# Kernel tuning notes

Hardware: AMD Instinct MI355X
Metric: run time of the kernel (lower is better)

Reference implementation:

```python
import jax, jax.numpy as jnp
import numpy as np

B = 8            # graphs per batch (batch_size)
NPG = 4096       # nodes per graph
EPG = 65536      # edges per graph (avg degree 16)
IN = 384
K1, K2, K3 = 2458, 1475, 738   # ceil(.6*4096), ceil(.6*2458), ceil(.5*1475)
EPS = 1e-5


def setup_inputs() -> dict:
    key = jax.random.key(0)
    ks = jax.random.split(key, 16)
    x = jax.random.normal(ks[0], (B * NPG, IN), jnp.float32)
    off = (jnp.arange(B, dtype=jnp.int32) * NPG)[:, None]
    src = jax.random.randint(ks[1], (B, EPG), 0, NPG, dtype=jnp.int32) + off
    dst = jax.random.randint(ks[2], (B, EPG), 0, NPG, dtype=jnp.int32) + off
    edge_index = jnp.stack([src.reshape(-1), dst.reshape(-1)])

    def lin(k, i, o):
        return jax.random.normal(k, (i, o), jnp.float32) / np.sqrt(i)

    return dict(
        x=x, edge_index=edge_index,
        W1=lin(ks[3], IN, 512), b1=jnp.zeros(512, jnp.float32),
        W2=lin(ks[4], 512, 512), b2=jnp.zeros(512, jnp.float32),
        W3=lin(ks[5], 512, 256), b3=jnp.zeros(256, jnp.float32),
        W4=lin(ks[6], 256, 192), b4=jnp.zeros(192, jnp.float32),
        g1=jnp.ones(512, jnp.float32), be1=jnp.zeros(512, jnp.float32),
        g2=jnp.ones(512, jnp.float32), be2=jnp.zeros(512, jnp.float32),
        g3=jnp.ones(256, jnp.float32), be3=jnp.zeros(256, jnp.float32),
        p1_wrel=lin(ks[7], 512, 1), p1_brel=jnp.zeros(1, jnp.float32), p1_wroot=lin(ks[8], 512, 1),
        p2_wrel=lin(ks[9], 512, 1), p2_brel=jnp.zeros(1, jnp.float32), p2_wroot=lin(ks[10], 512, 1),
        p3_wrel=lin(ks[11], 256, 1), p3_brel=jnp.zeros(1, jnp.float32), p3_wroot=lin(ks[12], 256, 1),
    )


def _gcn_conv(x, W, b, src, dst, em, n):
    # PyG GCNConv(add_self_loops=False): h = D^-1/2 A D^-1/2 (x W) + b
    h = x @ W
    deg = jax.ops.segment_sum(em, dst, num_segments=n)           # in-degree of valid edges
    dis = jnp.where(deg > 0, jax.lax.rsqrt(jnp.maximum(deg, 1e-12)), 0.0)
    norm = (dis[src] * dis[dst] * em)[:, None]
    return jax.ops.segment_sum(h[src] * norm, dst, num_segments=n) + b


def _bn(x, g, b):
    # BatchNorm(track_running_stats=False): always batch stats, biased var
    mu = jnp.mean(x, axis=0)
    var = jnp.mean(jnp.square(x - mu), axis=0)
    return (x - mu) * jax.lax.rsqrt(var + EPS) * g + b


def _sag_score(x, wrel, brel, wroot, src, dst, em, n):
    # SAGPooling's GNN = GraphConv: lin_rel(sum_j x_j) + lin_root(x)
    agg = jax.ops.segment_sum(x[src] * em[:, None], dst, num_segments=n)
    return (agg @ wrel + brel + x @ wroot)[:, 0]


def _sag_pool(x, score, src, dst, em, npg, k):
    # per-graph top-k on raw scores; kept features scaled by tanh(score)
    topv, topi = jax.lax.top_k(score.reshape(B, npg), k)
    perm = (topi + (jnp.arange(B, dtype=jnp.int32) * npg)[:, None]).reshape(-1)
    xn = x[perm] * jnp.tanh(topv.reshape(-1))[:, None]
    inv = jnp.full(B * npg, -1, jnp.int32).at[perm].set(
        jnp.arange(B * k, dtype=jnp.int32))
    ns, nd = inv[src], inv[dst]
    keep = (ns >= 0) & (nd >= 0)
    em = em * keep.astype(x.dtype)
    return xn, jnp.where(keep, ns, 0), jnp.where(keep, nd, 0), em


def reference(x, edge_index,
              W1, b1, W2, b2, W3, b3, W4, b4,
              g1, be1, g2, be2, g3, be3,
              p1_wrel, p1_brel, p1_wroot,
              p2_wrel, p2_brel, p2_wroot,
              p3_wrel, p3_brel, p3_wroot,
              batch_size=8):
    src, dst = edge_index[0], edge_index[1]
    em = jnp.ones(src.shape[0], x.dtype)

    h = jax.nn.relu(_bn(_gcn_conv(x, W1, b1, src, dst, em, B * NPG), g1, be1))
    s = _sag_score(h, p1_wrel, p1_brel, p1_wroot, src, dst, em, B * NPG)
    h, src, dst, em = _sag_pool(h, s, src, dst, em, NPG, K1)

    h = jax.nn.relu(_bn(_gcn_conv(h, W2, b2, src, dst, em, B * K1), g2, be2))
    s = _sag_score(h, p2_wrel, p2_brel, p2_wroot, src, dst, em, B * K1)
    h, src, dst, em = _sag_pool(h, s, src, dst, em, K1, K2)

    h = jax.nn.relu(_bn(_gcn_conv(h, W3, b3, src, dst, em, B * K2), g3, be3))
    s = _sag_score(h, p3_wrel, p3_brel, p3_wroot, src, dst, em, B * K2)
    h, src, dst, em = _sag_pool(h, s, src, dst, em, K2, K3)

    h = _gcn_conv(h, W4, b4, src, dst, em, B * K3)      # [B*K3, 192]
    hg = h.reshape(B, K3, 192)
    return jnp.mean(hg, axis=1) + jnp.max(hg, axis=1)   # global mean + max pool
```

## Files before the change

kernel.cpp:

```cpp
#include <hip/hip_runtime.h>
#include <cmath>

#define E_TOTAL 524288
#define NB 8

using f32x4 = __attribute__((ext_vector_type(4))) float;
using s16x8 = __attribute__((ext_vector_type(8))) short;
using s16x4 = __attribute__((ext_vector_type(4))) short;

static inline int cdiv(int a, int b) { return (a + b - 1) / b; }

__device__ inline unsigned short bf16_rn(float x) {
  unsigned u = __float_as_uint(x);
  return (unsigned short)((u + 0x7FFFu + ((u >> 16) & 1u)) >> 16);
}
__device__ inline void split3(float x, short& h, short& m, short& l) {
  unsigned short hb = bf16_rn(x);
  h = (short)hb;
  float hf = __uint_as_float(((unsigned)hb) << 16);
  float r1 = x - hf;
  unsigned short mb = bf16_rn(r1);
  m = (short)mb;
  float mf = __uint_as_float(((unsigned)mb) << 16);
  l = (short)bf16_rn(r1 - mf);
}

__global__ void fill_i32(int* p, int v, int n) {
  int i = blockIdx.x * 256 + threadIdx.x;
  if (i < n) p[i] = v;
}

__global__ void split_w_t(const float* __restrict__ W, short* __restrict__ TH,
                          short* __restrict__ TM, short* __restrict__ TL, int K, int N) {
  int i = blockIdx.x * 256 + threadIdx.x;
  if (i >= K * N) return;
  int k = i / N, n = i % N;
  short h, m, l;
  split3(W[i], h, m, l);
  TH[(size_t)n * K + k] = h;
  TM[(size_t)n * K + k] = m;
  TL[(size_t)n * K + k] = l;
}

#define GBM 128
#define GBN 128
#define GBK 32
#define ASTR 40

__global__ __launch_bounds__(256) void gemm_mfma(
    const short* __restrict__ AH, const short* __restrict__ AM, const short* __restrict__ AL,
    const short* __restrict__ BH, const short* __restrict__ BM, const short* __restrict__ BL,
    const float* __restrict__ bias, float* __restrict__ C,
    int M, int K, int N, int nblocks) {
  __shared__ __align__(16) short Ah[GBM * ASTR];
  __shared__ __align__(16) short Am[GBM * ASTR];
  __shared__ __align__(16) short Al[GBM * ASTR];
  __shared__ __align__(16) short Bh[GBN * ASTR];
  __shared__ __align__(16) short Bm[GBN * ASTR];
  __shared__ __align__(16) short Bl[GBN * ASTR];
  int nwg = gridDim.x;
  int orig = blockIdx.x;
  int q = nwg >> 3, r = nwg & 7;
  int xc = orig & 7, j8 = orig >> 3;
  int wg = (xc < r ? xc * (q + 1) : r * (q + 1) + (xc - r) * q) + j8;
  int bm = (wg / nblocks) * GBM;
  int bn = (wg % nblocks) * GBN;
  int tid = threadIdx.x;
  int wave = tid >> 6, lane = tid & 63;
  int wm = (wave >> 1) * 64, wn = (wave & 1) * 64;
  int l15 = lane & 15, l4 = lane >> 4;
  int arow = tid >> 1, ahalf = tid & 1;
  int garow = bm + arow;
  int gbcol = bn + arow;
  const bool avalid = garow < M;
  const bool bvalid = gbcol < N;
  int sw = (arow >> 3) & 3;
  int wofs0 = arow * ASTR + (((2 * ahalf) ^ sw) << 3);
  int wofs1 = arow * ASTR + (((2 * ahalf + 1) ^ sw) << 3);
  f32x4 acc[4][4] = {};
  for (int k0 = 0; k0 < K; k0 += GBK) {
    __syncthreads();
    {
      s16x8 z = {};
      size_t ga = (size_t)garow * K + k0 + ahalf * 16;
      size_t gb = (size_t)gbcol * K + k0 + ahalf * 16;
      s16x8 v0, v1;
      v0 = avalid ? *(const s16x8*)(AH + ga) : z;
      v1 = avalid ? *(const s16x8*)(AH + ga + 8) : z;
      *(s16x8*)&Ah[wofs0] = v0;  *(s16x8*)&Ah[wofs1] = v1;
      v0 = avalid ? *(const s16x8*)(AM + ga) : z;
      v1 = avalid ? *(const s16x8*)(AM + ga + 8) : z;
      *(s16x8*)&Am[wofs0] = v0;  *(s16x8*)&Am[wofs1] = v1;
      v0 = avalid ? *(const s16x8*)(AL + ga) : z;
      v1 = avalid ? *(const s16x8*)(AL + ga + 8) : z;
      *(s16x8*)&Al[wofs0] = v0;  *(s16x8*)&Al[wofs1] = v1;
      v0 = bvalid ? *(const s16x8*)(BH + gb) : z;
      v1 = bvalid ? *(const s16x8*)(BH + gb + 8) : z;
      *(s16x8*)&Bh[wofs0] = v0;  *(s16x8*)&Bh[wofs1] = v1;
      v0 = bvalid ? *(const s16x8*)(BM + gb) : z;
      v1 = bvalid ? *(const s16x8*)(BM + gb + 8) : z;
      *(s16x8*)&Bm[wofs0] = v0;  *(s16x8*)&Bm[wofs1] = v1;
      v0 = bvalid ? *(const s16x8*)(BL + gb) : z;
      v1 = bvalid ? *(const s16x8*)(BL + gb + 8) : z;
      *(s16x8*)&Bl[wofs0] = v0;  *(s16x8*)&Bl[wofs1] = v1;
    }
    __syncthreads();
    s16x8 fah[4], fam[4], fal[4], fbh[4], fbm[4], fbl[4];
#pragma unroll
    for (int mi = 0; mi < 4; ++mi) {
      int row = wm + mi * 16 + l15;
      int ad = row * ASTR + ((l4 ^ ((row >> 3) & 3)) << 3);
      fah[mi] = *(const s16x8*)&Ah[ad];
      fam[mi] = *(const s16x8*)&Am[ad];
      fal[mi] = *(const s16x8*)&Al[ad];
    }
#pragma unroll
    for (int ni = 0; ni < 4; ++ni) {
      int row = wn + ni * 16 + l15;
      int bd = row * ASTR + ((l4 ^ ((row >> 3) & 3)) << 3);
      fbh[ni] = *(const s16x8*)&Bh[bd];
      fbm[ni] = *(const s16x8*)&Bm[bd];
      fbl[ni] = *(const s16x8*)&Bl[bd];
    }
#pragma unroll
    for (int mi = 0; mi < 4; ++mi)
#pragma unroll
      for (int ni = 0; ni < 4; ++ni) {
        acc[mi][ni] = __builtin_amdgcn_mfma_f32_16x16x32_bf16(fah[mi], fbh[ni], acc[mi][ni], 0, 0, 0);
        acc[mi][ni] = __builtin_amdgcn_mfma_f32_16x16x32_bf16(fah[mi], fbm[ni], acc[mi][ni], 0, 0, 0);
        acc[mi][ni] = __builtin_amdgcn_mfma_f32_16x16x32_bf16(fam[mi], fbh[ni], acc[mi][ni], 0, 0, 0);
        acc[mi][ni] = __builtin_amdgcn_mfma_f32_16x16x32_bf16(fah[mi], fbl[ni], acc[mi][ni], 0, 0, 0);
        acc[mi][ni] = __builtin_amdgcn_mfma_f32_16x16x32_bf16(fal[mi], fbh[ni], acc[mi][ni], 0, 0, 0);
        acc[mi][ni] = __builtin_amdgcn_mfma_f32_16x16x32_bf16(fam[mi], fbm[ni], acc[mi][ni], 0, 0, 0);
      }
  }
#pragma unroll
  for (int ni = 0; ni < 4; ++ni) {
    int col = bn + wn + ni * 16 + l15;
    if (col >= N) continue;
    float bv = bias ? bias[col] : 0.f;
#pragma unroll
    for (int mi = 0; mi < 4; ++mi) {
      int row0 = bm + wm + mi * 16 + l4 * 4;
#pragma unroll
      for (int rr = 0; rr < 4; ++rr) {
        int row = row0 + rr;
        if (row < M) C[(size_t)row * N + col] = acc[mi][ni][rr] + bv;
      }
    }
  }
}

__global__ void count_kernel(const int* __restrict__ dst, int* __restrict__ cnt, int E) {
  int e = blockIdx.x * 256 + threadIdx.x;
  if (e >= E) return;
  atomicAdd(&cnt[dst[e]], 1);
}

__global__ __launch_bounds__(1024) void scan_kernel(const int* __restrict__ cnt,
                                                    int* __restrict__ offs, int n) {
  __shared__ int tsum[1024];
  int tid = threadIdx.x;
  int chunk = (n + 1023) / 1024;
  int base = tid * chunk;
  int lsum = 0;
  for (int i = 0; i < chunk; ++i) {
    int idx = base + i;
    if (idx < n) lsum += cnt[idx];
  }
  tsum[tid] = lsum;
  __syncthreads();
  for (int off = 1; off < 1024; off <<= 1) {
    int add = (tid >= off) ? tsum[tid - off] : 0;
    __syncthreads();
    tsum[tid] += add;
    __syncthreads();
  }
  int run = (tid == 0) ? 0 : tsum[tid - 1];
  for (int i = 0; i < chunk; ++i) {
    int idx = base + i;
    if (idx < n) { offs[idx] = run; run += cnt[idx]; }
  }
  if (tid == 1023) offs[n] = run;
}

__global__ void dis_kernel(const int* __restrict__ cnt, float* __restrict__ dis, int n) {
  int i = blockIdx.x * 256 + threadIdx.x;
  if (i >= n) return;
  int c = cnt[i];
  dis[i] = (c > 0) ? (float)(1.0 / sqrt((double)c)) : 0.f;
}

__global__ void scatter_kernel(const int* __restrict__ src, const int* __restrict__ dst,
                               const int* __restrict__ offs, int* __restrict__ tmpc,
                               int* __restrict__ esrc, int E) {
  int e = blockIdx.x * 256 + threadIdx.x;
  if (e >= E) return;
  int d = dst[e];
  if (d < 0) return;
  int pos = offs[d] + atomicAdd(&tmpc[d], 1);
  esrc[pos] = src[e];
}

__global__ void sort_buckets(const int* __restrict__ offs, int* __restrict__ esrc, int n) {
  int node = blockIdx.x * 256 + threadIdx.x;
  if (node >= n) return;
  int s0 = offs[node], s1 = offs[node + 1];
  for (int i = s0 + 1; i < s1; ++i) {
    int v = esrc[i];
    int j = i - 1;
    while (j >= s0 && esrc[j] > v) { esrc[j + 1] = esrc[j]; --j; }
    esrc[j + 1] = v;
  }
}

__global__ __launch_bounds__(256) void agg_kernel(
    const float* __restrict__ h, const int* __restrict__ offs,
    const int* __restrict__ esrc, const float* __restrict__ dis,
    const float* __restrict__ bias, float* __restrict__ outf,
    short* __restrict__ outh, short* __restrict__ outm, short* __restrict__ outl,
    int F, int n) {
  int node = blockIdx.x * 4 + (threadIdx.x >> 6);
  if (node >= n) return;
  int lane = threadIdx.x & 63;
  int nf4 = F >> 2;
  int i0 = lane, i1 = lane + 64;
  bool a0 = i0 < nf4, a1 = i1 < nf4;
  f32x4 acc0 = {}, acc1 = {};
  int e0 = offs[node], e1 = offs[node + 1];
  int e = e0;
  for (; e + 4 <= e1; e += 4) {
    int s0 = esrc[e], s1 = esrc[e + 1], s2 = esrc[e + 2], s3 = esrc[e + 3];
    float w0 = dis[s0], w1 = dis[s1], w2 = dis[s2], w3 = dis[s3];
    const f32x4* p0 = (const f32x4*)(h + (size_t)s0 * F);
    const f32x4* p1 = (const f32x4*)(h + (size_t)s1 * F);
    const f32x4* p2 = (const f32x4*)(h + (size_t)s2 * F);
    const f32x4* p3 = (const f32x4*)(h + (size_t)s3 * F);
    if (a0) {
      f32x4 v0 = p0[i0], v1 = p1[i0], v2 = p2[i0], v3 = p3[i0];
      acc0 += v0 * w0;
      acc0 += v1 * w1;
      acc0 += v2 * w2;
      acc0 += v3 * w3;
    }
    if (a1) {
      f32x4 v0 = p0[i1], v1 = p1[i1], v2 = p2[i1], v3 = p3[i1];
      acc1 += v0 * w0;
      acc1 += v1 * w1;
      acc1 += v2 * w2;
      acc1 += v3 * w3;
    }
  }
  for (; e < e1; ++e) {
    int s = esrc[e];
    float w = dis[s];
    const f32x4* hp = (const f32x4*)(h + (size_t)s * F);
    if (a0) acc0 += hp[i0] * w;
    if (a1) acc1 += hp[i1] * w;
  }
  float wd = dis[node];
  acc0 *= wd;
  acc1 *= wd;
  if (outf) {
    const f32x4* b4 = (const f32x4*)bias;
    f32x4* op = (f32x4*)(outf + (size_t)node * F);
    if (a0) op[i0] = acc0 + b4[i0];
    if (a1) op[i1] = acc1 + b4[i1];
  } else {
    short hh[4], mm[4], ll[4];
    if (a0) {
#pragma unroll
      for (int c = 0; c < 4; ++c) split3(acc0[c], hh[c], mm[c], ll[c]);
      *(s16x4*)&outh[(size_t)node * F + i0 * 4] = *(s16x4*)hh;
      *(s16x4*)&outm[(size_t)node * F + i0 * 4] = *(s16x4*)mm;
      *(s16x4*)&outl[(size_t)node * F + i0 * 4] = *(s16x4*)ll;
    }
    if (a1) {
#pragma unroll
      for (int c = 0; c < 4; ++c) split3(acc1[c], hh[c], mm[c], ll[c]);
      *(s16x4*)&outh[(size_t)node * F + i1 * 4] = *(s16x4*)hh;
      *(s16x4*)&outm[(size_t)node * F + i1 * 4] = *(s16x4*)mm;
      *(s16x4*)&outl[(size_t)node * F + i1 * 4] = *(s16x4*)ll;
    }
  }
}

#define BNY 512
__global__ void bn_stats_part(const float* __restrict__ x, double* __restrict__ psum,
                              double* __restrict__ psq, int n, int F) {
  int col = blockIdx.x * 256 + threadIdx.x;
  if (col >= F) return;
  double s = 0., q = 0.;
  for (int r = blockIdx.y; r < n; r += gridDim.y) {
    double v = (double)x[(size_t)r * F + col];
    s += v;
    q += v * v;
  }
  psum[blockIdx.y * F + col] = s;
  psq[blockIdx.y * F + col] = q;
}

__global__ __launch_bounds__(64) void bn_reduce(
    const double* __restrict__ psum, const double* __restrict__ psq,
    const float* __restrict__ g, const float* __restrict__ be,
    float* __restrict__ scf, float* __restrict__ shf,
    double* __restrict__ scd, double* __restrict__ shd, int n, int F) {
  int c = blockIdx.x;
  int lane = threadIdx.x;
  double s = 0., q = 0.;
  for (int p = lane; p < BNY; p += 64) {
    s += psum[p * F + c];
    q += psq[p * F + c];
  }
#pragma unroll
  for (int o = 1; o < 64; o <<= 1) {
    s += __shfl_xor(s, o, 64);
    q += __shfl_xor(q, o, 64);
  }
  if (lane == 0) {
    double inv_n = 1.0 / (double)n;
    double mu = s * inv_n;
    double var = q * inv_n - mu * mu;
    if (var < 0.) var = 0.;
    double istd = 1.0 / sqrt(var + 1e-5);
    double sc = istd * (double)g[c];
    double sh = (double)be[c] - mu * sc;
    scd[c] = sc;
    shd[c] = sh;
    scf[c] = (float)sc;
    shf[c] = (float)sh;
  }
}

__global__ __launch_bounds__(256) void bn_apply_score(
    float* __restrict__ hx, const float* __restrict__ scf, const float* __restrict__ shf,
    const double* __restrict__ scd, const double* __restrict__ shd,
    const float* __restrict__ wrel, const float* __restrict__ wroot,
    double* __restrict__ t, double* __restrict__ r, int F, int n) {
  int row = blockIdx.x * 4 + (threadIdx.x >> 6);
  if (row >= n) return;
  int lane = threadIdx.x & 63;
  int nf4 = F >> 2;
  f32x4* hp = (f32x4*)(hx + (size_t)row * F);
  const f32x4* sc = (const f32x4*)scf;
  const f32x4* sh = (const f32x4*)shf;
  double dr = 0., dq = 0.;
  for (int j = lane; j < nf4; j += 64) {
    f32x4 hv = hp[j];
    f32x4 v = hv * sc[j] + sh[j];
#pragma unroll
    for (int c = 0; c < 4; ++c) v[c] = fmaxf(v[c], 0.f);
    hp[j] = v;
#pragma unroll
    for (int c = 0; c < 4; ++c) {
      double vd = (double)hv[c] * scd[j * 4 + c] + shd[j * 4 + c];
      vd = vd > 0. ? vd : 0.;
      dr += vd * (double)wrel[j * 4 + c];
      dq += vd * (double)wroot[j * 4 + c];
    }
  }
#pragma unroll
  for (int o = 1; o < 64; o <<= 1) {
    dr += __shfl_xor(dr, o, 64);
    dq += __shfl_xor(dq, o, 64);
  }
  if (lane == 0) { t[row] = dr; r[row] = dq; }
}

__global__ void score_kernel(const int* __restrict__ offs, const int* __restrict__ esrc,
                             const double* __restrict__ t, const double* __restrict__ r,
                             const float* __restrict__ brel, double* __restrict__ s, int n) {
  int i = blockIdx.x * 256 + threadIdx.x;
  if (i >= n) return;
  double acc = 0.;
  int e0 = offs[i], e1 = offs[i + 1];
  for (int e = e0; e < e1; ++e) acc += t[esrc[e]];
  s[i] = acc + r[i] + (double)brel[0];
}

__global__ __launch_bounds__(1024) void topk_kernel(
    const double* __restrict__ s, int n_pg, int k, int npad,
    int* __restrict__ perm, float* __restrict__ tanhv, int* __restrict__ inv) {
  extern __shared__ char smem[];
  unsigned long long* sk = (unsigned long long*)smem;
  unsigned* si = (unsigned*)(smem + (size_t)npad * 8);
  int g = blockIdx.x;
  for (int i = threadIdx.x; i < npad; i += blockDim.x) {
    if (i < n_pg) {
      double v = s[(size_t)g * n_pg + i];
      unsigned long long u = (unsigned long long)__double_as_longlong(v);
      u = (u >> 63) ? ~u : (u | 0x8000000000000000ULL);
      sk[i] = ~u;
      si[i] = (unsigned)i;
    } else {
      sk[i] = 0xFFFFFFFFFFFFFFFFULL;
      si[i] = 0xFFFFFFFFu;
    }
  }
  __syncthreads();
  for (int size = 2; size <= npad; size <<= 1) {
    for (int stride = size >> 1; stride > 0; stride >>= 1) {
      for (int t = threadIdx.x; t < (npad >> 1); t += blockDim.x) {
        int i = ((t / stride) * stride * 2) + (t % stride);
        int j = i + stride;
        bool up = ((i & size) == 0);
        unsigned long long ka = sk[i], kb = sk[j];
        unsigned ia = si[i], ib = si[j];
        bool sw = up ? ((ka > kb) || (ka == kb && ia > ib))
                     : ((ka < kb) || (ka == kb && ia < ib));
        if (sw) { sk[i] = kb; sk[j] = ka; si[i] = ib; si[j] = ia; }
      }
      __syncthreads();
    }
  }
  for (int j = threadIdx.x; j < k; j += blockDim.x) {
    int li = (int)si[j];
    int old_g = g * n_pg + li;
    int new_g = g * k + j;
    perm[new_g] = old_g;
    tanhv[new_g] = (float)tanh(s[old_g]);
    inv[old_g] = new_g;
  }
}

__global__ __launch_bounds__(256) void gather_split(
    const float* __restrict__ h, const int* __restrict__ perm,
    const float* __restrict__ tanhv, short* __restrict__ gh, short* __restrict__ gm,
    short* __restrict__ gl, int F, int nk) {
  int i = blockIdx.x * 4 + (threadIdx.x >> 6);
  if (i >= nk) return;
  int lane = threadIdx.x & 63;
  int nf4 = F >> 2;
  int p = perm[i];
  float tv = tanhv[i];
  const f32x4* hp = (const f32x4*)(h + (size_t)p * F);
  for (int j = lane; j < nf4; j += 64) {
    f32x4 v = hp[j] * tv;
    short hh[4], mm[4], ll[4];
#pragma unroll
    for (int c = 0; c < 4; ++c) split3(v[c], hh[c], mm[c], ll[c]);
    *(s16x4*)&gh[(size_t)i * F + j * 4] = *(s16x4*)hh;
    *(s16x4*)&gm[(size_t)i * F + j * 4] = *(s16x4*)mm;
    *(s16x4*)&gl[(size_t)i * F + j * 4] = *(s16x4*)ll;
  }
}

__global__ void remap_kernel(const int* __restrict__ src_in, const int* __restrict__ dst_in,
                             const int* __restrict__ inv, int* __restrict__ src_out,
                             int* __restrict__ dst_out, int* __restrict__ cnt, int E) {
  int e = blockIdx.x * 256 + threadIdx.x;
  if (e >= E) return;
  int d = dst_in[e];
  int ns = -1, nd = -1;
  if (d >= 0) { ns = inv[src_in[e]]; nd = inv[d]; }
  if (ns >= 0 && nd >= 0) {
    src_out[e] = ns;
    dst_out[e] = nd;
    atomicAdd(&cnt[nd], 1);
  } else {
    src_out[e] = 0;
    dst_out[e] = -1;
  }
}

#define PCH 16
__global__ void pool_partial(const float* __restrict__ h, float* __restrict__ part,
                             int k3, int F) {
  int g = blockIdx.x, c = blockIdx.y;
  int tid = threadIdx.x;
  int chunk = (k3 + PCH - 1) / PCH;
  int r0 = c * chunk, r1 = min(r0 + chunk, k3);
  const float* base = h + (size_t)g * k3 * F;
  float sm = 0.f, mx = -INFINITY;
  for (int r = r0; r < r1; ++r) {
    float v = base[(size_t)r * F + tid];
    sm += v;
    mx = fmaxf(mx, v);
  }
  float* pp = part + (size_t)(g * PCH + c) * 2 * F;
  pp[tid] = sm;
  pp[F + tid] = mx;
}
__global__ void pool_final(const float* __restrict__ part, float* __restrict__ out,
                           int k3, int F) {
  int g = blockIdx.x;
  int tid = threadIdx.x;
  float sm = 0.f, mx = -INFINITY;
  for (int c = 0; c < PCH; ++c) {
    const float* pp = part + (size_t)(g * PCH + c) * 2 * F;
    sm += pp[tid];
    mx = fmaxf(mx, pp[F + tid]);
  }
  out[g * F + tid] = sm / (float)k3 + mx;
}

extern "C" void kernel_launch(void* const* d_in, const int* in_sizes, int n_in,
                              void* d_out, int out_size, void* d_ws, size_t ws_size,
                              hipStream_t stream) {
  const float* x0 = (const float*)d_in[0];
  const int* eidx = (const int*)d_in[1];
  const float* W1 = (const float*)d_in[2];  const float* b1 = (const float*)d_in[3];
  const float* W2 = (const float*)d_in[4];  const float* b2 = (const float*)d_in[5];
  const float* W3 = (const float*)d_in[6];  const float* b3 = (const float*)d_in[7];
  const float* W4 = (const float*)d_in[8];  const float* b4 = (const float*)d_in[9];
  const float* g1 = (const float*)d_in[10]; const float* be1 = (const float*)d_in[11];
  const float* g2 = (const float*)d_in[12]; const float* be2 = (const float*)d_in[13];
  const float* g3 = (const float*)d_in[14]; const float* be3 = (const float*)d_in[15];
  const float* p1r = (const float*)d_in[16]; const float* p1b = (const float*)d_in[17];
  const float* p1o = (const float*)d_in[18];
  const float* p2r = (const float*)d_in[19]; const float* p2b = (const float*)d_in[20];
  const float* p2o = (const float*)d_in[21];
  const float* p3r = (const float*)d_in[22]; const float* p3b = (const float*)d_in[23];
  const float* p3o = (const float*)d_in[24];

  char* w = (char*)d_ws;
  size_t off = 0;
  auto alloc = [&](size_t bytes) -> void* {
    void* p = w + off;
    off = (off + bytes + 255) & ~(size_t)255;
    return p;
  };
  float* BUF0 = (float*)alloc(32768ull * 512 * 4);
  float* BUF1 = (float*)alloc(19664ull * 512 * 4);
  short* XH = (short*)alloc(32768ull * 384 * 2);
  short* XM = (short*)alloc(32768ull * 384 * 2);
  short* XL = (short*)alloc(32768ull * 384 * 2);
  short* WTH = (short*)alloc(638976ull * 2);
  short* WTM = (short*)alloc(638976ull * 2);
  short* WTL = (short*)alloc(638976ull * 2);
  int* czone = (int*)alloc(65537ull * 4);
  int* cnt = czone;
  int* tmpc = czone + 32769;
  int* offs = (int*)alloc(32769 * 4);
  float* dis = (float*)alloc(32768 * 4);
  double* tvec = (double*)alloc(32768 * 8);
  double* rvec = (double*)alloc(32768 * 8);
  double* svec = (double*)alloc(32768 * 8);
  int* inv = (int*)alloc(32768 * 4);
  int* perm = (int*)alloc(32768 * 4);
  float* tanhv = (float*)alloc(32768 * 4);
  int* e0s = (int*)alloc(E_TOTAL * 4);
  int* e0d = (int*)alloc(E_TOTAL * 4);
  int* e1s = (int*)alloc(E_TOTAL * 4);
  int* e1d = (int*)alloc(E_TOTAL * 4);
  int* esrc = (int*)alloc(E_TOTAL * 4);
  double* bnsum = (double*)alloc((size_t)BNY * 512 * 8);
  double* bnsq = (double*)alloc((size_t)BNY * 512 * 8);
  float* bnscf = (float*)alloc(512 * 4);
  float* bnshf = (float*)alloc(512 * 4);
  double* bnscd = (double*)alloc(512 * 8);
  double* bnshd = (double*)alloc(512 * 8);
  float* part = (float*)alloc((size_t)NB * PCH * 2 * 192 * 4);

  const int EB = cdiv(E_TOTAL, 256);

  auto build_csr = [&](const int* src, const int* dst, int n) {
    scan_kernel<<<1, 1024, 0, stream>>>(cnt, offs, n);
    dis_kernel<<<cdiv(n, 256), 256, 0, stream>>>(cnt, dis, n);
    scatter_kernel<<<EB, 256, 0, stream>>>(src, dst, offs, tmpc, esrc, E_TOTAL);
    sort_buckets<<<cdiv(n, 256), 256, 0, stream>>>(offs, esrc, n);
  };

  auto pool = [&](float* hbuf, int n, int n_pg, int k, int npad, int F,
                  const float* g, const float* be, const float* wr, const float* wb,
                  const float* wo, const int* src, const int* dst, int* nsrc, int* ndst) {
    bn_stats_part<<<dim3(cdiv(F, 256), BNY), 256, 0, stream>>>(hbuf, bnsum, bnsq, n, F);
    bn_reduce<<<F, 64, 0, stream>>>(bnsum, bnsq, g, be, bnscf, bnshf, bnscd, bnshd, n, F);
    bn_apply_score<<<cdiv(n, 4), 256, 0, stream>>>(hbuf, bnscf, bnshf, bnscd, bnshd, wr, wo, tvec, rvec, F, n);
    score_kernel<<<cdiv(n, 256), 256, 0, stream>>>(offs, esrc, tvec, rvec, wb, svec, n);
    fill_i32<<<cdiv(n, 256), 256, 0, stream>>>(inv, -1, n);
    topk_kernel<<<NB, 1024, (size_t)npad * 12, stream>>>(svec, n_pg, k, npad, perm, tanhv, inv);
    gather_split<<<cdiv(NB * k, 4), 256, 0, stream>>>(hbuf, perm, tanhv, XH, XM, XL, F, NB * k);
    fill_i32<<<cdiv(65537, 256), 256, 0, stream>>>(czone, 0, 65537);
    remap_kernel<<<EB, 256, 0, stream>>>(src, dst, inv, nsrc, ndst, cnt, E_TOTAL);
  };

  split_w_t<<<cdiv(384 * 512, 256), 256, 0, stream>>>(W1, WTH, WTM, WTL, 384, 512);
  split_w_t<<<cdiv(512 * 512, 256), 256, 0, stream>>>(W2, WTH + 196608, WTM + 196608, WTL + 196608, 512, 512);
  split_w_t<<<cdiv(512 * 256, 256), 256, 0, stream>>>(W3, WTH + 458752, WTM + 458752, WTL + 458752, 512, 256);
  split_w_t<<<cdiv(256 * 192, 256), 256, 0, stream>>>(W4, WTH + 589824, WTM + 589824, WTL + 589824, 256, 192);

  fill_i32<<<cdiv(65537, 256), 256, 0, stream>>>(czone, 0, 65537);
  count_kernel<<<EB, 256, 0, stream>>>(eidx + E_TOTAL, cnt, E_TOTAL);
  build_csr(eidx, eidx + E_TOTAL, 32768);
  agg_kernel<<<cdiv(32768, 4), 256, 0, stream>>>(x0, offs, esrc, dis, nullptr, nullptr, XH, XM, XL, 384, 32768);
  gemm_mfma<<<cdiv(32768, 128) * 4, 256, 0, stream>>>(XH, XM, XL, WTH, WTM, WTL, b1, BUF0, 32768, 384, 512, 4);
  pool(BUF0, 32768, 4096, 2458, 4096, 512, g1, be1, p1r, p1b, p1o, eidx, eidx + E_TOTAL, e0s, e0d);

  build_csr(e0s, e0d, 19664);
  gemm_mfma<<<cdiv(19664, 128) * 4, 256, 0, stream>>>(XH, XM, XL, WTH + 196608, WTM + 196608, WTL + 196608, nullptr, BUF0, 19664, 512, 512, 4);
  agg_kernel<<<cdiv(19664, 4), 256, 0, stream>>>(BUF0, offs, esrc, dis, b2, BUF1, nullptr, nullptr, nullptr, 512, 19664);
  pool(BUF1, 19664, 2458, 1475, 4096, 512, g2, be2, p2r, p2b, p2o, e0s, e0d, e1s, e1d);

  build_csr(e1s, e1d, 11800);
  gemm_mfma<<<cdiv(11800, 128) * 2, 256, 0, stream>>>(XH, XM, XL, WTH + 458752, WTM + 458752, WTL + 458752, nullptr, BUF0, 11800, 512, 256, 2);
  agg_kernel<<<cdiv(11800, 4), 256, 0, stream>>>(BUF0, offs, esrc, dis, b3, BUF1, nullptr, nullptr, nullptr, 256, 11800);
  pool(BUF1, 11800, 1475, 738, 2048, 256, g3, be3, p3r, p3b, p3o, e1s, e1d, e0s, e0d);

  build_csr(e0s, e0d, 5904);
  gemm_mfma<<<cdiv(5904, 128) * 2, 256, 0, stream>>>(XH, XM, XL, WTH + 589824, WTM + 589824, WTL + 589824, nullptr, BUF0, 5904, 256, 192, 2);
  agg_kernel<<<cdiv(5904, 4), 256, 0, stream>>>(BUF0, offs, esrc, dis, b4, BUF1, nullptr, nullptr, nullptr, 192, 5904);
  pool_partial<<<dim3(NB, PCH), 192, 0, stream>>>(BUF1, part, 738, 192);
  pool_final<<<NB, 192, 0, stream>>>(part, (float*)d_out, 738, 192);
}
```

Before: 1.185 ms.

## Load GEMM fragments directly from global memory and fold dis into scan

The MFMA GEMM no longer stages A/B tiles through shared memory with barriers. Each wave now loads its bf16 split fragments straight from global memory into registers. This removes LDS traffic and __syncthreads, but it drops reuse of each tile across waves, so every wave refetches the same data from cache. Separately, the dis_kernel launch is removed and the inverse-sqrt degree is computed inside the single-block scan, saving one launch per CSR build.

```diff
diff --git a/kernel.cpp b/kernel.cpp
--- a/kernel.cpp
+++ b/kernel.cpp
@@ -45,19 +45,12 @@
 #define GBM 128
 #define GBN 128
 #define GBK 32
-#define ASTR 40
 
 __global__ __launch_bounds__(256) void gemm_mfma(
     const short* __restrict__ AH, const short* __restrict__ AM, const short* __restrict__ AL,
     const short* __restrict__ BH, const short* __restrict__ BM, const short* __restrict__ BL,
     const float* __restrict__ bias, float* __restrict__ C,
     int M, int K, int N, int nblocks) {
-  __shared__ __align__(16) short Ah[GBM * ASTR];
-  __shared__ __align__(16) short Am[GBM * ASTR];
-  __shared__ __align__(16) short Al[GBM * ASTR];
-  __shared__ __align__(16) short Bh[GBN * ASTR];
-  __shared__ __align__(16) short Bm[GBN * ASTR];
-  __shared__ __align__(16) short Bl[GBN * ASTR];
   int nwg = gridDim.x;
   int orig = blockIdx.x;
   int q = nwg >> 3, r = nwg & 7;
@@ -69,58 +62,37 @@
   int wave = tid >> 6, lane = tid & 63;
   int wm = (wave >> 1) * 64, wn = (wave & 1) * 64;
   int l15 = lane & 15, l4 = lane >> 4;
-  int arow = tid >> 1, ahalf = tid & 1;
-  int garow = bm + arow;
-  int gbcol = bn + arow;
-  const bool avalid = garow < M;
-  const bool bvalid = gbcol < N;
-  int sw = (arow >> 3) & 3;
-  int wofs0 = arow * ASTR + (((2 * ahalf) ^ sw) << 3);
-  int wofs1 = arow * ASTR + (((2 * ahalf + 1) ^ sw) << 3);
+  size_t abase[4], bbase[4];
+  bool av[4], bv[4];
+#pragma unroll
+  for (int mi = 0; mi < 4; ++mi) {
+    int row = bm + wm + mi * 16 + l15;
+    av[mi] = row < M;
+    abase[mi] = (size_t)(av[mi] ? row : 0) * K + l4 * 8;
+  }
+#pragma unroll
+  for (int ni = 0; ni < 4; ++ni) {
+    int col = bn + wn + ni * 16 + l15;
+    bv[ni] = col < N;
+    bbase[ni] = (size_t)(bv[ni] ? col : 0) * K + l4 * 8;
+  }
   f32x4 acc[4][4] = {};
+  const s16x8 z = {};
   for (int k0 = 0; k0 < K; k0 += GBK) {
-    __syncthreads();
-    {
-      s16x8 z = {};
-      size_t ga = (size_t)garow * K + k0 + ahalf * 16;
-      size_t gb = (size_t)gbcol * K + k0 + ahalf * 16;
-      s16x8 v0, v1;
-      v0 = avalid ? *(const s16x8*)(AH + ga) : z;
-      v1 = avalid ? *(const s16x8*)(AH + ga + 8) : z;
-      *(s16x8*)&Ah[wofs0] = v0;  *(s16x8*)&Ah[wofs1] = v1;
-      v0 = avalid ? *(const s16x8*)(AM + ga) : z;
-      v1 = avalid ? *(const s16x8*)(AM + ga + 8) : z;
-      *(s16x8*)&Am[wofs0] = v0;  *(s16x8*)&Am[wofs1] = v1;
-      v0 = avalid ? *(const s16x8*)(AL + ga) : z;
-      v1 = avalid ? *(const s16x8*)(AL + ga + 8) : z;
-      *(s16x8*)&Al[wofs0] = v0;  *(s16x8*)&Al[wofs1] = v1;
-      v0 = bvalid ? *(const s16x8*)(BH + gb) : z;
-      v1 = bvalid ? *(const s16x8*)(BH + gb + 8) : z;
-      *(s16x8*)&Bh[wofs0] = v0;  *(s16x8*)&Bh[wofs1] = v1;
-      v0 = bvalid ? *(const s16x8*)(BM + gb) : z;
-      v1 = bvalid ? *(const s16x8*)(BM + gb + 8) : z;
-      *(s16x8*)&Bm[wofs0] = v0;  *(s16x8*)&Bm[wofs1] = v1;
-      v0 = bvalid ? *(const s16x8*)(BL + gb) : z;
-      v1 = bvalid ? *(const s16x8*)(BL + gb + 8) : z;
-      *(s16x8*)&Bl[wofs0] = v0;  *(s16x8*)&Bl[wofs1] = v1;
-    }
-    __syncthreads();
     s16x8 fah[4], fam[4], fal[4], fbh[4], fbm[4], fbl[4];
 #pragma unroll
     for (int mi = 0; mi < 4; ++mi) {
-      int row = wm + mi * 16 + l15;
-      int ad = row * ASTR + ((l4 ^ ((row >> 3) & 3)) << 3);
-      fah[mi] = *(const s16x8*)&Ah[ad];
-      fam[mi] = *(const s16x8*)&Am[ad];
-      fal[mi] = *(const s16x8*)&Al[ad];
+      size_t a = abase[mi] + k0;
+      fah[mi] = av[mi] ? *(const s16x8*)(AH + a) : z;
+      fam[mi] = av[mi] ? *(const s16x8*)(AM + a) : z;
+      fal[mi] = av[mi] ? *(const s16x8*)(AL + a) : z;
     }
 #pragma unroll
     for (int ni = 0; ni < 4; ++ni) {
-      int row = wn + ni * 16 + l15;
-      int bd = row * ASTR + ((l4 ^ ((row >> 3) & 3)) << 3);
-      fbh[ni] = *(const s16x8*)&Bh[bd];
-      fbm[ni] = *(const s16x8*)&Bm[bd];
-      fbl[ni] = *(const s16x8*)&Bl[bd];
+      size_t b = bbase[ni] + k0;
+      fbh[ni] = bv[ni] ? *(const s16x8*)(BH + b) : z;
+      fbm[ni] = bv[ni] ? *(const s16x8*)(BM + b) : z;
+      fbl[ni] = bv[ni] ? *(const s16x8*)(BL + b) : z;
     }
 #pragma unroll
     for (int mi = 0; mi < 4; ++mi)
@@ -138,14 +110,14 @@
   for (int ni = 0; ni < 4; ++ni) {
     int col = bn + wn + ni * 16 + l15;
     if (col >= N) continue;
-    float bv = bias ? bias[col] : 0.f;
+    float bvv = bias ? bias[col] : 0.f;
 #pragma unroll
     for (int mi = 0; mi < 4; ++mi) {
       int row0 = bm + wm + mi * 16 + l4 * 4;
 #pragma unroll
       for (int rr = 0; rr < 4; ++rr) {
         int row = row0 + rr;
-        if (row < M) C[(size_t)row * N + col] = acc[mi][ni][rr] + bv;
+        if (row < M) C[(size_t)row * N + col] = acc[mi][ni][rr] + bvv;
       }
     }
   }
@@ -158,7 +130,8 @@
 }
 
 __global__ __launch_bounds__(1024) void scan_kernel(const int* __restrict__ cnt,
-                                                    int* __restrict__ offs, int n) {
+                                                    int* __restrict__ offs,
+                                                    float* __restrict__ dis, int n) {
   __shared__ int tsum[1024];
   int tid = threadIdx.x;
   int chunk = (n + 1023) / 1024;
@@ -179,16 +152,14 @@
   int run = (tid == 0) ? 0 : tsum[tid - 1];
   for (int i = 0; i < chunk; ++i) {
     int idx = base + i;
-    if (idx < n) { offs[idx] = run; run += cnt[idx]; }
+    if (idx < n) {
+      offs[idx] = run;
+      int c = cnt[idx];
+      run += c;
+      dis[idx] = (c > 0) ? (float)(1.0 / sqrt((double)c)) : 0.f;
+    }
   }
   if (tid == 1023) offs[n] = run;
-}
-
-__global__ void dis_kernel(const int* __restrict__ cnt, float* __restrict__ dis, int n) {
-  int i = blockIdx.x * 256 + threadIdx.x;
-  if (i >= n) return;
-  int c = cnt[i];
-  dis[i] = (c > 0) ? (float)(1.0 / sqrt((double)c)) : 0.f;
 }
 
 __global__ void scatter_kernel(const int* __restrict__ src, const int* __restrict__ dst,
@@ -555,8 +526,7 @@
   const int EB = cdiv(E_TOTAL, 256);
 
   auto build_csr = [&](const int* src, const int* dst, int n) {
-    scan_kernel<<<1, 1024, 0, stream>>>(cnt, offs, n);
-    dis_kernel<<<cdiv(n, 256), 256, 0, stream>>>(cnt, dis, n);
+    scan_kernel<<<1, 1024, 0, stream>>>(cnt, offs, dis, n);
     scatter_kernel<<<EB, 256, 0, stream>>>(src, dst, offs, tmpc, esrc, E_TOTAL);
     sort_buckets<<<cdiv(n, 256), 256, 0, stream>>>(offs, esrc, n);
   };
```

After: 1.310 ms. +10.6%, slower.
